# Performance work log

Hardware: AMD Instinct MI355X
Metric: run time of the kernel (lower is better)

Reference implementation:

```python
import jax, jax.numpy as jnp
import numpy as np

MARGIN = 0.3
N, D, N_IDS = 8192, 128, 1024


def setup_inputs() -> dict:
    key = jax.random.key(0)
    k1, k2 = jax.random.split(key)
    inputs = jax.random.normal(k1, (N, D), dtype=jnp.float32)
    targets = jax.random.randint(k2, (N,), 0, N_IDS)
    return {"inputs": inputs, "targets": targets}


def reference(inputs, targets):
    # mask[i, j] = True iff sample j shares sample i's identity (includes j == i)
    mask = targets[:, None] == targets[None, :]               # [n, n] bool
    maskf = mask.astype(inputs.dtype)
    counts = maskf.sum(axis=1, keepdims=True)                 # [n, 1] (>= 1, self match)
    # center_i = mean of positives of sample i
    centers = (maskf @ inputs) / counts                       # [n, d]
    # squared distance from every center i to every sample j via gram expansion
    x2 = jnp.sum(inputs * inputs, axis=1)                     # [n]
    c2 = jnp.sum(centers * centers, axis=1)                   # [n]
    dist2 = c2[:, None] + x2[None, :] - 2.0 * (centers @ inputs.T)  # [n, n]
    # hard mining: farthest positive from center, closest negative to center
    dist_cp = jnp.where(mask, dist2, -jnp.inf).max(axis=1)    # [n]
    dist_cn = jnp.where(mask, jnp.inf, dist2).min(axis=1)     # [n]
    # MarginRankingLoss(y=1): mean(relu(-(dist_cn - dist_cp) + margin))
    loss = jnp.mean(jax.nn.relu(dist_cp - dist_cn + MARGIN))
    prec = jnp.mean((dist_cn > dist_cp).astype(jnp.float32))
    return loss, prec
```

## Files before the change

kernel.cpp:

```cpp
#include <hip/hip_runtime.h>
#include <math.h>

#define N_SAMPLES 8192
#define DIM 128
#define NCLS 1024
#define MARGIN_V 0.3f
#define DIST_GX (N_SAMPLES / 128)
#define DIST_GY (NCLS / 64)
#define NPART DIST_GX
#define MAXMEM 64
#define PIPE 16

using bf16x8 = __attribute__((ext_vector_type(8))) short;
using f32x16 = __attribute__((ext_vector_type(16))) float;
using short8 = __attribute__((ext_vector_type(8))) short;

__device__ __forceinline__ short bf16_rne(float x) {
  unsigned u = __float_as_uint(x);
  unsigned r = u + 0x7FFFu + ((u >> 16) & 1u);
  return (short)(r >> 16);
}

__device__ __forceinline__ size_t frag_idx(int row, int oct) {
  int tile = row >> 5, ks = oct >> 1, lane = ((oct & 1) << 5) | (row & 31);
  return (size_t)(tile * 8 + ks) * 64 + lane;
}

__global__ __launch_bounds__(256) void pack_kernel(
    const float* __restrict__ inputs, const int* __restrict__ targets,
    float* __restrict__ x2, float* __restrict__ c2, int* __restrict__ counts,
    short8* __restrict__ Apk, short8* __restrict__ Bpk, float* __restrict__ out) {
  int b = blockIdx.x;
  int tid = threadIdx.x;
  if (b == 0 && tid < 2) out[tid] = 0.f;
  if (b < N_SAMPLES / 16) {
    int row = b * 16 + (tid >> 4);
    int oct = tid & 15;
    const float4* p = (const float4*)(inputs + (size_t)row * DIM + oct * 8);
    float4 v0 = p[0], v1 = p[1];
    float v[8] = {v0.x, v0.y, v0.z, v0.w, v1.x, v1.y, v1.z, v1.w};
    float s = 0.f;
    #pragma unroll
    for (int i = 0; i < 8; i++) s += v[i] * v[i];
    #pragma unroll
    for (int m = 1; m < 16; m <<= 1) s += __shfl_xor(s, m);
    if (oct == 0) x2[row] = s;
    short8 hi;
    #pragma unroll
    for (int i = 0; i < 8; i++) hi[i] = bf16_rne(v[i]);
    Bpk[frag_idx(row, oct)] = hi;
  } else {
    __shared__ int mem[2][MAXMEM];
    __shared__ int mcnt[2];
    __shared__ float sctr[2][128];
    __shared__ float wsum[4];
    int c0 = (b - N_SAMPLES / 16) * 2;
    if (tid < 2) { mcnt[tid] = 0; mem[tid][0] = 0; }
    __syncthreads();
    int tg[N_SAMPLES / 256];
    #pragma unroll
    for (int i = 0; i < N_SAMPLES / 256; i++) tg[i] = targets[tid + 256 * i];
    #pragma unroll
    for (int i = 0; i < N_SAMPLES / 256; i++) {
      if (tg[i] == c0) {
        int p = atomicAdd(&mcnt[0], 1);
        if (p < MAXMEM) mem[0][p] = tid + 256 * i;
      } else if (tg[i] == c0 + 1) {
        int p = atomicAdd(&mcnt[1], 1);
        if (p < MAXMEM) mem[1][p] = tid + 256 * i;
      }
    }
    __syncthreads();
    int half = tid >> 7;
    int c = c0 + half;
    int d = tid & 127;
    int cnt = mcnt[half];
    int cl = (cnt < MAXMEM) ? cnt : MAXMEM;
    int n1 = (cl < PIPE) ? cl : PIPE;
    int idxs[PIPE];
    #pragma unroll
    for (int i = 0; i < PIPE; i++) idxs[i] = mem[half][(i < n1) ? i : 0];
    float vbuf[PIPE];
    #pragma unroll
    for (int i = 0; i < PIPE; i++) vbuf[i] = inputs[(size_t)idxs[i] * DIM + d];
    float acc = 0.f;
    #pragma unroll
    for (int i = 0; i < PIPE; i++) if (i < n1) acc += vbuf[i];
    for (int m = PIPE; m < cl; m++) acc += inputs[(size_t)mem[half][m] * DIM + d];
    float ctrv = (cnt > 0) ? acc / (float)cnt : 0.f;
    sctr[half][d] = ctrv;
    float vv = ctrv * ctrv;
    #pragma unroll
    for (int sh = 32; sh > 0; sh >>= 1) vv += __shfl_down(vv, sh);
    if ((tid & 63) == 0) wsum[tid >> 6] = vv;
    __syncthreads();
    if (d == 0) {
      c2[c] = wsum[half * 2] + wsum[half * 2 + 1];
      counts[c] = cnt;
    }
    if (d < 16) {
      int oct = d;
      short8 hi;
      #pragma unroll
      for (int i = 0; i < 8; i++) hi[i] = bf16_rne(sctr[half][oct * 8 + i]);
      Apk[frag_idx(c, oct)] = hi;
    }
  }
}

__global__ __launch_bounds__(256, 3) void dist_kernel(
    const short8* __restrict__ Apk, const short8* __restrict__ Bpk,
    const float* __restrict__ x2, const float* __restrict__ c2,
    const int* __restrict__ targets,
    float* __restrict__ dp_part, float* __restrict__ dn_part) {
  __shared__ float sc2[64];
  __shared__ float sx2[128];
  __shared__ int stgt[128];
  __shared__ float redp[2][2][32];
  __shared__ float redn[2][2][32];

  int tid = threadIdx.x;
  int jbase = blockIdx.x * 128;
  int cbase = blockIdx.y * 64;
  int wave = tid >> 6, lane = tid & 63;
  int wm = wave >> 1, wn = wave & 1;

  if (tid < 128) {
    sx2[tid] = x2[jbase + tid];
    stgt[tid] = targets[jbase + tid];
  }
  if (tid < 64) sc2[tid] = c2[cbase + tid];

  int mtg = (cbase >> 5) + wm;
  int ntg0 = (jbase >> 5) + wn * 2;

  const short8* abase  = &Apk[(size_t)(mtg * 8) * 64 + lane];
  const short8* b0base = &Bpk[(size_t)((ntg0 + 0) * 8) * 64 + lane];
  const short8* b1base = &Bpk[(size_t)((ntg0 + 1) * 8) * 64 + lane];
  bf16x8 av[8], b0[8], b1[8];
  #pragma unroll
  for (int ks = 0; ks < 8; ks++) {
    av[ks] = abase[(size_t)ks * 64];
    b0[ks] = b0base[(size_t)ks * 64];
    b1[ks] = b1base[(size_t)ks * 64];
  }

  f32x16 acc[2];
  acc[0] = (f32x16)(0.f);
  acc[1] = (f32x16)(0.f);

  #pragma unroll
  for (int ks = 0; ks < 8; ks++) {
    acc[0] = __builtin_amdgcn_mfma_f32_32x32x16_bf16(b0[ks], av[ks], acc[0], 0, 0, 0);
    acc[1] = __builtin_amdgcn_mfma_f32_32x32x16_bf16(b1[ks], av[ks], acc[1], 0, 0, 0);
  }

  __syncthreads();

  int col = lane & 31;
  int hf = lane >> 5;
  int c_loc = wm * 32 + col;
  int cg = cbase + c_loc;
  float c2v = sc2[c_loc];
  float pmax = -INFINITY, nmin = INFINITY;
  #pragma unroll
  for (int nt = 0; nt < 2; nt++) {
    #pragma unroll
    for (int r = 0; r < 16; r++) {
      int j_loc = wn * 64 + nt * 32 + (r & 3) + 8 * (r >> 2) + 4 * hf;
      float d2 = c2v + sx2[j_loc] - 2.f * acc[nt][r];
      if (stgt[j_loc] == cg) pmax = fmaxf(pmax, d2);
      else                   nmin = fminf(nmin, d2);
    }
  }
  pmax = fmaxf(pmax, __shfl_xor(pmax, 32));
  nmin = fminf(nmin, __shfl_xor(nmin, 32));
  if (lane < 32) {
    redp[wn][wm][col] = pmax;
    redn[wn][wm][col] = nmin;
  }
  __syncthreads();
  if (tid < 64) {
    int wmx = tid >> 5, idx = tid & 31;
    float dp = fmaxf(redp[0][wmx][idx], redp[1][wmx][idx]);
    float dn = fminf(redn[0][wmx][idx], redn[1][wmx][idx]);
    size_t slot = (size_t)blockIdx.x * NCLS + cbase + tid;
    dp_part[slot] = dp;
    dn_part[slot] = dn;
  }
}

__global__ __launch_bounds__(256) void finalize_kernel(
    const float* __restrict__ dp_part, const float* __restrict__ dn_part,
    const int* __restrict__ counts, float* __restrict__ out) {
  __shared__ float sdp[4][64];
  __shared__ float sdn[4][64];
  int g = blockIdx.x;
  int t = threadIdx.x;
  int cl = t & 63;
  int pg = t >> 6;
  int c = g * 64 + cl;
  float dp = -INFINITY, dn = INFINITY;
  #pragma unroll
  for (int p = pg * 16; p < pg * 16 + 16; p++) {
    dp = fmaxf(dp, dp_part[(size_t)p * NCLS + c]);
    dn = fminf(dn, dn_part[(size_t)p * NCLS + c]);
  }
  sdp[pg][cl] = dp;
  sdn[pg][cl] = dn;
  __syncthreads();
  if (t < 64) {
    dp = fmaxf(fmaxf(sdp[0][cl], sdp[1][cl]), fmaxf(sdp[2][cl], sdp[3][cl]));
    dn = fminf(fminf(sdn[0][cl], sdn[1][cl]), fminf(sdn[2][cl], sdn[3][cl]));
    int cnt = counts[c];
    float ls = 0.f, ps = 0.f;
    if (cnt > 0) {
      ls = (float)cnt * fmaxf(dp - dn + MARGIN_V, 0.f);
      ps = (float)cnt * ((dn > dp) ? 1.f : 0.f);
    }
    #pragma unroll
    for (int sh = 32; sh > 0; sh >>= 1) {
      ls += __shfl_down(ls, sh);
      ps += __shfl_down(ps, sh);
    }
    if (t == 0) {
      atomicAdd(&out[0], ls / (float)N_SAMPLES);
      atomicAdd(&out[1], ps / (float)N_SAMPLES);
    }
  }
}

extern "C" void kernel_launch(void* const* d_in, const int* in_sizes, int n_in,
                              void* d_out, int out_size, void* d_ws, size_t ws_size,
                              hipStream_t stream) {
  const float* inputs = (const float*)d_in[0];
  const int* targets = (const int*)d_in[1];
  float* out = (float*)d_out;

  char* w = (char*)d_ws;
  float* x2 = (float*)w;            w += (size_t)N_SAMPLES * 4;
  float* c2 = (float*)w;            w += (size_t)NCLS * 4;
  int* counts = (int*)w;            w += (size_t)NCLS * 4;
  float* dp_part = (float*)w;       w += (size_t)NPART * NCLS * 4;
  float* dn_part = (float*)w;       w += (size_t)NPART * NCLS * 4;
  short8* Apk = (short8*)w;         w += (size_t)NCLS * DIM * 2;
  short8* Bpk = (short8*)w;         w += (size_t)N_SAMPLES * DIM * 2;

  pack_kernel<<<N_SAMPLES / 16 + NCLS / 2, 256, 0, stream>>>(
      inputs, targets, x2, c2, counts, Apk, Bpk, out);
  dist_kernel<<<dim3(DIST_GX, DIST_GY), 256, 0, stream>>>(
      Apk, Bpk, x2, c2, targets, dp_part, dn_part);
  finalize_kernel<<<16, 256, 0, stream>>>(dp_part, dn_part, counts, out);
}
```

Before: 69.88 us.

## Fuse finalize into dist kernel via last-block atomic counter; vectorize target loads

Removes the separate finalize launch by having each dist block bump a global atomic counter, with the last block to finish doing the cross-partition max/min reduction and writing the loss and precision. This saves one kernel launch and its dependency gap, but leaves a single block serially reducing all 16 class groups, plus a fence and atomic in every block. Separately, the class-membership scan in pack_kernel now loads targets as int4 instead of scalar ints.

```diff
diff --git a/kernel.cpp b/kernel.cpp
--- a/kernel.cpp
+++ b/kernel.cpp
@@ -8,6 +8,7 @@
 #define DIST_GX (N_SAMPLES / 128)
 #define DIST_GY (NCLS / 64)
 #define NPART DIST_GX
+#define NBLK (DIST_GX * DIST_GY)
 #define MAXMEM 64
 #define PIPE 16
 
@@ -29,10 +30,10 @@
 __global__ __launch_bounds__(256) void pack_kernel(
     const float* __restrict__ inputs, const int* __restrict__ targets,
     float* __restrict__ x2, float* __restrict__ c2, int* __restrict__ counts,
-    short8* __restrict__ Apk, short8* __restrict__ Bpk, float* __restrict__ out) {
+    short8* __restrict__ Apk, short8* __restrict__ Bpk, int* __restrict__ ctr) {
   int b = blockIdx.x;
   int tid = threadIdx.x;
-  if (b == 0 && tid < 2) out[tid] = 0.f;
+  if (b == 0 && tid == 0) ctr[0] = 0;
   if (b < N_SAMPLES / 16) {
     int row = b * 16 + (tid >> 4);
     int oct = tid & 15;
@@ -57,17 +58,23 @@
     int c0 = (b - N_SAMPLES / 16) * 2;
     if (tid < 2) { mcnt[tid] = 0; mem[tid][0] = 0; }
     __syncthreads();
-    int tg[N_SAMPLES / 256];
-    #pragma unroll
-    for (int i = 0; i < N_SAMPLES / 256; i++) tg[i] = targets[tid + 256 * i];
-    #pragma unroll
-    for (int i = 0; i < N_SAMPLES / 256; i++) {
-      if (tg[i] == c0) {
-        int p = atomicAdd(&mcnt[0], 1);
-        if (p < MAXMEM) mem[0][p] = tid + 256 * i;
-      } else if (tg[i] == c0 + 1) {
-        int p = atomicAdd(&mcnt[1], 1);
-        if (p < MAXMEM) mem[1][p] = tid + 256 * i;
+    const int4* tv = (const int4*)targets;
+    int4 tg[8];
+    #pragma unroll
+    for (int q = 0; q < 8; q++) tg[q] = tv[tid + 256 * q];
+    #pragma unroll
+    for (int q = 0; q < 8; q++) {
+      int base = 4 * (tid + 256 * q);
+      int te[4] = {tg[q].x, tg[q].y, tg[q].z, tg[q].w};
+      #pragma unroll
+      for (int e = 0; e < 4; e++) {
+        if (te[e] == c0) {
+          int p = atomicAdd(&mcnt[0], 1);
+          if (p < MAXMEM) mem[0][p] = base + e;
+        } else if (te[e] == c0 + 1) {
+          int p = atomicAdd(&mcnt[1], 1);
+          if (p < MAXMEM) mem[1][p] = base + e;
+        }
       }
     }
     __syncthreads();
@@ -111,13 +118,17 @@
 __global__ __launch_bounds__(256, 3) void dist_kernel(
     const short8* __restrict__ Apk, const short8* __restrict__ Bpk,
     const float* __restrict__ x2, const float* __restrict__ c2,
-    const int* __restrict__ targets,
-    float* __restrict__ dp_part, float* __restrict__ dn_part) {
+    const int* __restrict__ targets, const int* __restrict__ counts,
+    float* __restrict__ dp_part, float* __restrict__ dn_part,
+    int* __restrict__ ctr, float* __restrict__ out) {
   __shared__ float sc2[64];
   __shared__ float sx2[128];
   __shared__ int stgt[128];
   __shared__ float redp[2][2][32];
   __shared__ float redn[2][2][32];
+  __shared__ float sdp[4][64];
+  __shared__ float sdn[4][64];
+  __shared__ int s_last;
 
   int tid = threadIdx.x;
   int jbase = blockIdx.x * 128;
@@ -188,44 +199,52 @@
     dp_part[slot] = dp;
     dn_part[slot] = dn;
   }
-}
-
-__global__ __launch_bounds__(256) void finalize_kernel(
-    const float* __restrict__ dp_part, const float* __restrict__ dn_part,
-    const int* __restrict__ counts, float* __restrict__ out) {
-  __shared__ float sdp[4][64];
-  __shared__ float sdn[4][64];
-  int g = blockIdx.x;
-  int t = threadIdx.x;
-  int cl = t & 63;
-  int pg = t >> 6;
-  int c = g * 64 + cl;
-  float dp = -INFINITY, dn = INFINITY;
-  #pragma unroll
-  for (int p = pg * 16; p < pg * 16 + 16; p++) {
-    dp = fmaxf(dp, dp_part[(size_t)p * NCLS + c]);
-    dn = fminf(dn, dn_part[(size_t)p * NCLS + c]);
-  }
-  sdp[pg][cl] = dp;
-  sdn[pg][cl] = dn;
-  __syncthreads();
-  if (t < 64) {
-    dp = fmaxf(fmaxf(sdp[0][cl], sdp[1][cl]), fmaxf(sdp[2][cl], sdp[3][cl]));
-    dn = fminf(fminf(sdn[0][cl], sdn[1][cl]), fminf(sdn[2][cl], sdn[3][cl]));
-    int cnt = counts[c];
-    float ls = 0.f, ps = 0.f;
-    if (cnt > 0) {
-      ls = (float)cnt * fmaxf(dp - dn + MARGIN_V, 0.f);
-      ps = (float)cnt * ((dn > dp) ? 1.f : 0.f);
-    }
+
+  __syncthreads();
+  if (tid == 0) {
+    __threadfence();
+    int prev = __hip_atomic_fetch_add(ctr, 1, __ATOMIC_ACQ_REL,
+                                      __HIP_MEMORY_SCOPE_AGENT);
+    s_last = (prev == NBLK - 1) ? 1 : 0;
+  }
+  __syncthreads();
+  if (!s_last) return;
+  __threadfence();
+
+  float ls_acc = 0.f, ps_acc = 0.f;
+  for (int g = 0; g < 16; g++) {
+    int cl = tid & 63;
+    int pg = tid >> 6;
+    int c = g * 64 + cl;
+    float dp = -INFINITY, dn = INFINITY;
+    #pragma unroll
+    for (int p = pg * 16; p < pg * 16 + 16; p++) {
+      dp = fmaxf(dp, dp_part[(size_t)p * NCLS + c]);
+      dn = fminf(dn, dn_part[(size_t)p * NCLS + c]);
+    }
+    sdp[pg][cl] = dp;
+    sdn[pg][cl] = dn;
+    __syncthreads();
+    if (tid < 64) {
+      float dpf = fmaxf(fmaxf(sdp[0][tid], sdp[1][tid]), fmaxf(sdp[2][tid], sdp[3][tid]));
+      float dnf = fminf(fminf(sdn[0][tid], sdn[1][tid]), fminf(sdn[2][tid], sdn[3][tid]));
+      int cnt = counts[g * 64 + tid];
+      if (cnt > 0) {
+        ls_acc += (float)cnt * fmaxf(dpf - dnf + MARGIN_V, 0.f);
+        ps_acc += (float)cnt * ((dnf > dpf) ? 1.f : 0.f);
+      }
+    }
+    __syncthreads();
+  }
+  if (tid < 64) {
     #pragma unroll
     for (int sh = 32; sh > 0; sh >>= 1) {
-      ls += __shfl_down(ls, sh);
-      ps += __shfl_down(ps, sh);
-    }
-    if (t == 0) {
-      atomicAdd(&out[0], ls / (float)N_SAMPLES);
-      atomicAdd(&out[1], ps / (float)N_SAMPLES);
+      ls_acc += __shfl_down(ls_acc, sh);
+      ps_acc += __shfl_down(ps_acc, sh);
+    }
+    if (tid == 0) {
+      out[0] = ls_acc / (float)N_SAMPLES;
+      out[1] = ps_acc / (float)N_SAMPLES;
     }
   }
 }
@@ -238,6 +257,7 @@
   float* out = (float*)d_out;
 
   char* w = (char*)d_ws;
+  int* ctr = (int*)w;               w += 16;
   float* x2 = (float*)w;            w += (size_t)N_SAMPLES * 4;
   float* c2 = (float*)w;            w += (size_t)NCLS * 4;
   int* counts = (int*)w;            w += (size_t)NCLS * 4;
@@ -247,8 +267,7 @@
   short8* Bpk = (short8*)w;         w += (size_t)N_SAMPLES * DIM * 2;
 
   pack_kernel<<<N_SAMPLES / 16 + NCLS / 2, 256, 0, stream>>>(
-      inputs, targets, x2, c2, counts, Apk, Bpk, out);
+      inputs, targets, x2, c2, counts, Apk, Bpk, ctr);
   dist_kernel<<<dim3(DIST_GX, DIST_GY), 256, 0, stream>>>(
-      Apk, Bpk, x2, c2, targets, dp_part, dn_part);
-  finalize_kernel<<<16, 256, 0, stream>>>(dp_part, dn_part, counts, out);
-}
+      Apk, Bpk, x2, c2, targets, counts, dp_part, dn_part, ctr, out);
+}
```

New measurement: 169.7 us. 2.43x slower.
